# Kernel optimization log

Measured on AMD Instinct MI355X. Metric: run time of the kernel, lower is better.

The kernel has to match this reference:

```python
import jax, jax.numpy as jnp
import numpy as np

# dims
N, E, HID = 20000, 320000, 128
L, H = 12, 4            # num_layers, heads
C = 2 * HID             # h width = in_channels = out_channels*heads = 256
OC = C // H             # per-head out channels = 64
FF = 4 * HID            # ffn hidden = 512
LN_EPS = 1e-5
SLOPE = 0.2             # GATConv leaky_relu negative slope


def _layer_norm(x, g, b):
    m = x.mean(-1, keepdims=True)
    v = ((x - m) ** 2).mean(-1, keepdims=True)
    return (x - m) * jax.lax.rsqrt(v + LN_EPS) * g + b


def setup_inputs() -> dict:
    key = jax.random.key(0)
    ks = jax.random.split(key, 16)
    s = 0.05
    f32 = jnp.float32
    return {
        "hf": jax.random.normal(ks[0], (N, HID), f32),
        "hs": jax.random.normal(ks[1], (N, HID), f32),
        "edge_index": jax.random.randint(ks[2], (2, E), 0, N, dtype=jnp.int32),
        # GATConv params (stacked over layers)
        "W": jax.random.normal(ks[3], (L, C, H * OC), f32) * s,       # lin (no bias)
        "att_src": jax.random.normal(ks[4], (L, H, OC), f32) * s,
        "att_dst": jax.random.normal(ks[5], (L, H, OC), f32) * s,
        "gat_b": jax.random.normal(ks[6], (L, C), f32) * s,            # GATConv bias
        # FFN params
        "w1": jax.random.normal(ks[7], (L, C, FF), f32) * s,
        "b1": jax.random.normal(ks[8], (L, FF), f32) * s,
        "w2": jax.random.normal(ks[9], (L, FF, C), f32) * s,
        "b2": jax.random.normal(ks[10], (L, C), f32) * s,
        # LayerNorm params
        "ln1_g": jnp.ones((L, C), f32),
        "ln1_b": jnp.zeros((L, C), f32),
        "ln2_g": jnp.ones((L, C), f32),
        "ln2_b": jnp.zeros((L, C), f32),
    }


def reference(hf, hs, edge_index, W, att_src, att_dst, gat_b,
              w1, b1, w2, b2, ln1_g, ln1_b, ln2_g, ln2_b):
    # PyG GATConv add_self_loops=True
    loop = jnp.arange(N, dtype=edge_index.dtype)
    src = jnp.concatenate([edge_index[0], loop])  # [E+N]
    dst = jnp.concatenate([edge_index[1], loop])

    h = jnp.concatenate([hf, hs], axis=-1)  # [N, C]
    for i in range(L):
        # --- GATConv + residual + LN (dropout = identity at eval) ---
        r = h
        xh = (h @ W[i]).reshape(N, H, OC)              # [N,H,OC]
        a_s = (xh * att_src[i]).sum(-1)                # [N,H]
        a_d = (xh * att_dst[i]).sum(-1)                # [N,H]
        e = jax.nn.leaky_relu(a_s[src] + a_d[dst], SLOPE)          # [E+N,H]
        m = jax.ops.segment_max(e, dst, num_segments=N)            # [N,H]
        ex = jnp.exp(e - m[dst])
        z = jax.ops.segment_sum(ex, dst, num_segments=N)           # [N,H]
        alpha = ex / z[dst]                                        # segment softmax
        msg = xh[src] * alpha[..., None]                           # [E+N,H,OC]
        out = jax.ops.segment_sum(msg, dst, num_segments=N).reshape(N, C) + gat_b[i]
        h = _layer_norm(out + r, ln1_g[i], ln1_b[i])
        # --- FFN + residual + LN ---
        r = h
        f = jax.nn.relu(h @ w1[i] + b1[i]) @ w2[i] + b2[i]
        h = _layer_norm(f + r, ln2_g[i], ln2_b[i])

    return h[:, :HID], h[:, HID:]
```

## Files before the change

kernel.cpp:

```cpp
#include <hip/hip_runtime.h>
#include <hip/hip_bf16.h>
#include <math.h>

#define C_DIM 256
#define HID 128
#define HEADS 4
#define OC 64
#define FF_DIM 512
#define NLAYERS 12

constexpr float LN_EPS = 1e-5f;
constexpr float SLOPE  = 0.2f;

typedef __attribute__((ext_vector_type(4))) float f32x4;
typedef __attribute__((ext_vector_type(8))) short bf16x8_t;
typedef __attribute__((ext_vector_type(4))) int i32x4;

__device__ __forceinline__ float leaky(float x) { return x > 0.f ? x : SLOPE * x; }

__device__ __forceinline__ float bf2f(unsigned short u) {
    union { unsigned i; float f; } v; v.i = ((unsigned)u) << 16; return v.f;
}
__device__ __forceinline__ void bf2x(unsigned u, float& lo, float& hi) {
    union { unsigned i; float f; } a, b;
    a.i = u << 16; b.i = u & 0xffff0000u;
    lo = a.f; hi = b.f;
}
__device__ __forceinline__ unsigned packbf(float lo, float hi) {
    unsigned a = __bfloat16_as_ushort(__float2bfloat16(lo));
    unsigned b = __bfloat16_as_ushort(__float2bfloat16(hi));
    return a | (b << 16);
}

__global__ void zero_i32_kernel(int* __restrict__ p, int n) {
    int i = blockIdx.x * blockDim.x + threadIdx.x;
    if (i < n) p[i] = 0;
}

__global__ void concat_kernel(const float* __restrict__ hf, const float* __restrict__ hs,
                              __hip_bfloat16* __restrict__ hb, int Nn) {
    int idx = blockIdx.x * blockDim.x + threadIdx.x;
    int total = Nn * C_DIM;
    if (idx < total) {
        int n = idx >> 8;
        int c = idx & 255;
        float v = (c < HID) ? hf[n * HID + c] : hs[n * HID + (c - HID)];
        hb[idx] = __float2bfloat16(v);
    }
}

__global__ void transp_bf16_kernel(const float* __restrict__ in,
                                   __hip_bfloat16* __restrict__ out, int K, int N) {
    __shared__ float t[32][33];
    const float* inl = in + (size_t)blockIdx.z * K * N;
    __hip_bfloat16* outl = out + (size_t)blockIdx.z * K * N;
    int kb = blockIdx.y * 32, nb = blockIdx.x * 32;
    int tx = threadIdx.x & 31, ty = threadIdx.x >> 5;
    #pragma unroll
    for (int r = 0; r < 32; r += 8)
        t[ty + r][tx] = inl[(size_t)(kb + ty + r) * N + nb + tx];
    __syncthreads();
    #pragma unroll
    for (int r = 0; r < 32; r += 8)
        outl[(size_t)(nb + ty + r) * K + kb + tx] = __float2bfloat16(t[tx][ty + r]);
}

__global__ void hist_kernel(const int* __restrict__ dst, int* __restrict__ counts, int E) {
    int e = blockIdx.x * blockDim.x + threadIdx.x;
    if (e < E) atomicAdd(&counts[dst[e]], 1);
}

__global__ void scan_kernel(const int* __restrict__ counts, int* __restrict__ offsets,
                            int* __restrict__ cursor, int n) {
    __shared__ int wsum[16];
    __shared__ int carry_s;
    const int lane = threadIdx.x & 63, wid = threadIdx.x >> 6;
    if (threadIdx.x == 0) carry_s = 0;
    __syncthreads();
    for (int base = 0; base < n; base += 1024) {
        int i = base + (int)threadIdx.x;
        int v = (i < n) ? counts[i] : 0;
        int x = v;
        #pragma unroll
        for (int off = 1; off < 64; off <<= 1) {
            int t = __shfl_up(x, off);
            if (lane >= off) x += t;
        }
        if (lane == 63) wsum[wid] = x;
        __syncthreads();
        if (threadIdx.x == 0) {
            int acc = carry_s;
            #pragma unroll
            for (int w = 0; w < 16; ++w) { int t = wsum[w]; wsum[w] = acc; acc += t; }
            carry_s = acc;
        }
        __syncthreads();
        int excl = wsum[wid] + x - v;
        if (i < n) { offsets[i] = excl; cursor[i] = excl; }
        __syncthreads();
    }
    if (threadIdx.x == 0) offsets[n] = carry_s;
}

__global__ void fill_kernel(const int* __restrict__ src, const int* __restrict__ dst,
                            int* __restrict__ cursor, int* __restrict__ csr_src, int E) {
    int e = blockIdx.x * blockDim.x + threadIdx.x;
    if (e < E) {
        int d = dst[e];
        int p = atomicAdd(&cursor[d], 1);
        csr_src[p] = src[e];
    }
}

#define GBM 64
#define GBN 64
#define GBK 64
#define GLS 72

__global__ __launch_bounds__(256) void gemm_bf16_kernel(
    const __hip_bfloat16* __restrict__ A,
    const __hip_bfloat16* __restrict__ BT,
    const float* __restrict__ bias,
    __hip_bfloat16* __restrict__ Cb,
    const float* __restrict__ attS,
    const float* __restrict__ attD,
    float* __restrict__ aS,
    float* __restrict__ aD,
    int M, int N, int K, int relu)
{
    __shared__ short As[GBM * GLS];
    __shared__ short Bs[GBN * GLS];
    __shared__ float attP[2][2][GBM];
    const int tid = threadIdx.x;
    const int wave = tid >> 6, lane = tid & 63;
    const int lr = lane & 15, lq = lane >> 4;
    const int wm = (wave >> 1) * 32, wn = (wave & 1) * 32;
    const int row0 = blockIdx.x * GBM, col0 = blockIdx.y * GBN;

    const int sr = tid >> 2;
    const int sc = (tid & 3) * 16;

    f32x4 acc[2][2] = {};

    for (int k0 = 0; k0 < K; k0 += GBK) {
        int gr = row0 + sr;
        i32x4 va0 = {}, va1 = {};
        if (gr < M) {
            const __hip_bfloat16* ap = &A[(size_t)gr * K + k0 + sc];
            va0 = *(const i32x4*)ap;
            va1 = *(const i32x4*)(ap + 8);
        }
        *(i32x4*)&As[sr * GLS + sc] = va0;
        *(i32x4*)&As[sr * GLS + sc + 8] = va1;
        const __hip_bfloat16* bp = &BT[(size_t)(col0 + sr) * K + k0 + sc];
        *(i32x4*)&Bs[sr * GLS + sc] = *(const i32x4*)bp;
        *(i32x4*)&Bs[sr * GLS + sc + 8] = *(const i32x4*)(bp + 8);
        __syncthreads();

        #pragma unroll
        for (int ks = 0; ks < 2; ++ks) {
            bf16x8_t af[2], bfr[2];
            #pragma unroll
            for (int t = 0; t < 2; ++t) {
                af[t]  = *(const bf16x8_t*)&As[(wm + t * 16 + lr) * GLS + ks * 32 + lq * 8];
                bfr[t] = *(const bf16x8_t*)&Bs[(wn + t * 16 + lr) * GLS + ks * 32 + lq * 8];
            }
            #pragma unroll
            for (int mt = 0; mt < 2; ++mt)
                #pragma unroll
                for (int nt = 0; nt < 2; ++nt)
                    acc[mt][nt] = __builtin_amdgcn_mfma_f32_16x16x32_bf16(
                        af[mt], bfr[nt], acc[mt][nt], 0, 0, 0);
        }
        __syncthreads();
    }

    float bv[2];
    #pragma unroll
    for (int nt = 0; nt < 2; ++nt)
        bv[nt] = bias ? bias[col0 + wn + nt * 16 + lr] : 0.f;

    #pragma unroll
    for (int mt = 0; mt < 2; ++mt) {
        #pragma unroll
        for (int r = 0; r < 4; ++r) {
            int grow = row0 + wm + mt * 16 + lq * 4 + r;
            if (grow >= M) continue;
            #pragma unroll
            for (int nt = 0; nt < 2; ++nt) {
                float v = acc[mt][nt][r] + bv[nt];
                if (relu) v = fmaxf(v, 0.f);
                Cb[(size_t)grow * N + col0 + wn + nt * 16 + lr] = __float2bfloat16(v);
            }
        }
    }

    if (aS) {
        const int head = col0 >> 6;
        float atS[2], atD[2];
        #pragma unroll
        for (int nt = 0; nt < 2; ++nt) {
            int c = col0 + wn + nt * 16 + lr;
            atS[nt] = attS[c];
            atD[nt] = attD[c];
        }
        #pragma unroll
        for (int mt = 0; mt < 2; ++mt) {
            #pragma unroll
            for (int r = 0; r < 4; ++r) {
                float vs = acc[mt][0][r] * atS[0] + acc[mt][1][r] * atS[1];
                float vd = acc[mt][0][r] * atD[0] + acc[mt][1][r] * atD[1];
                #pragma unroll
                for (int off = 1; off < 16; off <<= 1) {
                    vs += __shfl_xor(vs, off);
                    vd += __shfl_xor(vd, off);
                }
                if (lr == 0) {
                    int rl = wm + mt * 16 + lq * 4 + r;
                    attP[wave & 1][0][rl] = vs;
                    attP[wave & 1][1][rl] = vd;
                }
            }
        }
        __syncthreads();
        if (tid < GBM) {
            int grow = row0 + tid;
            if (grow < M) {
                aS[grow * HEADS + head] = attP[0][0][tid] + attP[1][0][tid];
                aD[grow * HEADS + head] = attP[0][1][tid] + attP[1][1][tid];
            }
        }
    }
}

__global__ __launch_bounds__(256) void agg_kernel(
    const __hip_bfloat16* __restrict__ xhb, const float* __restrict__ a_s,
    const float* __restrict__ a_d, const int* __restrict__ csr,
    const int* __restrict__ offs, const float* __restrict__ gat_b,
    const float* __restrict__ ln_g, const float* __restrict__ ln_b,
    __hip_bfloat16* __restrict__ hb, int Nn)
{
    const int lane = threadIdx.x & 63;
    const int n = __builtin_amdgcn_readfirstlane(blockIdx.x * 4 + (threadIdx.x >> 6));
    if (n >= Nn) return;
    const int half = lane >> 5;
    const int sl = lane & 31;
    const int head = sl >> 3;
    const int c0 = sl * 8;
    const unsigned* x = (const unsigned*)xhb;
    const size_t rowp = (size_t)n * (C_DIM / 2) + (c0 >> 1);

    const float ad = a_d[n * 4 + head];

    const int beg = offs[n], end = offs[n + 1];
    const int ne = end - beg;
    const int nh0 = (ne + 1) >> 1;
    int ih  = half ? (beg + nh0) : beg;
    int cnt = half ? (ne - nh0) : nh0;

    i32x4 rv = *(const i32x4*)&((const unsigned*)hb)[rowp];

    float acc[8] = {};
    float z = 0.f;

    {
        float wself = __expf(leaky(a_s[n * 4 + head] + ad));
        if (half) {
            i32x4 xv = *(const i32x4*)&x[rowp];
            #pragma unroll
            for (int q = 0; q < 4; ++q) {
                float lo, hi; bf2x((unsigned)xv[q], lo, hi);
                acc[2 * q]     = wself * lo;
                acc[2 * q + 1] = wself * hi;
            }
            z = wself;
        }
    }

    for (; cnt >= 4; cnt -= 4, ih += 4) {
        int s0 = csr[ih], s1 = csr[ih + 1], s2 = csr[ih + 2], s3 = csr[ih + 3];
        float w0 = __expf(leaky(a_s[s0 * 4 + head] + ad));
        float w1 = __expf(leaky(a_s[s1 * 4 + head] + ad));
        float w2 = __expf(leaky(a_s[s2 * 4 + head] + ad));
        float w3 = __expf(leaky(a_s[s3 * 4 + head] + ad));
        i32x4 x0 = *(const i32x4*)&x[(size_t)s0 * (C_DIM / 2) + (c0 >> 1)];
        i32x4 x1 = *(const i32x4*)&x[(size_t)s1 * (C_DIM / 2) + (c0 >> 1)];
        i32x4 x2 = *(const i32x4*)&x[(size_t)s2 * (C_DIM / 2) + (c0 >> 1)];
        i32x4 x3 = *(const i32x4*)&x[(size_t)s3 * (C_DIM / 2) + (c0 >> 1)];
        #pragma unroll
        for (int q = 0; q < 4; ++q) {
            float lo, hi;
            bf2x((unsigned)x0[q], lo, hi);
            acc[2 * q] += w0 * lo; acc[2 * q + 1] += w0 * hi;
            bf2x((unsigned)x1[q], lo, hi);
            acc[2 * q] += w1 * lo; acc[2 * q + 1] += w1 * hi;
            bf2x((unsigned)x2[q], lo, hi);
            acc[2 * q] += w2 * lo; acc[2 * q + 1] += w2 * hi;
            bf2x((unsigned)x3[q], lo, hi);
            acc[2 * q] += w3 * lo; acc[2 * q + 1] += w3 * hi;
        }
        z += (w0 + w1) + (w2 + w3);
    }
    for (; cnt > 0; --cnt, ++ih) {
        int s0 = csr[ih];
        float w0 = __expf(leaky(a_s[s0 * 4 + head] + ad));
        i32x4 x0 = *(const i32x4*)&x[(size_t)s0 * (C_DIM / 2) + (c0 >> 1)];
        #pragma unroll
        for (int q = 0; q < 4; ++q) {
            float lo, hi; bf2x((unsigned)x0[q], lo, hi);
            acc[2 * q] += w0 * lo; acc[2 * q + 1] += w0 * hi;
        }
        z += w0;
    }

    #pragma unroll
    for (int j = 0; j < 8; ++j) acc[j] += __shfl_xor(acc[j], 32);
    z += __shfl_xor(z, 32);

    float res[8];
    #pragma unroll
    for (int q = 0; q < 4; ++q) bf2x((unsigned)rv[q], res[2 * q], res[2 * q + 1]);

    float4 gb0 = *(const float4*)&gat_b[c0];
    float4 gb1 = *(const float4*)&gat_b[c0 + 4];
    float gb[8] = {gb0.x, gb0.y, gb0.z, gb0.w, gb1.x, gb1.y, gb1.z, gb1.w};
    float rz = 1.0f / z;
    float val[8];
    #pragma unroll
    for (int j = 0; j < 8; ++j) val[j] = acc[j] * rz + gb[j] + res[j];

    float s1 = 0.f, s2 = 0.f;
    #pragma unroll
    for (int j = 0; j < 8; ++j) { s1 += val[j]; s2 += val[j] * val[j]; }
    #pragma unroll
    for (int off = 1; off < 64; off <<= 1) {
        s1 += __shfl_xor(s1, off);
        s2 += __shfl_xor(s2, off);
    }
    float mean = s1 * (1.0f / (2 * C_DIM));
    float inv = rsqrtf(s2 * (1.0f / (2 * C_DIM)) - mean * mean + LN_EPS);

    if (half == 0) {
        float4 g0 = *(const float4*)&ln_g[c0];
        float4 g1 = *(const float4*)&ln_g[c0 + 4];
        float4 bb0 = *(const float4*)&ln_b[c0];
        float4 bb1 = *(const float4*)&ln_b[c0 + 4];
        float g[8] = {g0.x, g0.y, g0.z, g0.w, g1.x, g1.y, g1.z, g1.w};
        float bb[8] = {bb0.x, bb0.y, bb0.z, bb0.w, bb1.x, bb1.y, bb1.z, bb1.w};
        float o[8];
        #pragma unroll
        for (int j = 0; j < 8; ++j) o[j] = (val[j] - mean) * inv * g[j] + bb[j];
        i32x4 ob;
        ob[0] = (int)packbf(o[0], o[1]);
        ob[1] = (int)packbf(o[2], o[3]);
        ob[2] = (int)packbf(o[4], o[5]);
        ob[3] = (int)packbf(o[6], o[7]);
        *(i32x4*)&((unsigned*)hb)[rowp] = ob;
    }
}

__global__ __launch_bounds__(256) void ln2_kernel(
    const __hip_bfloat16* __restrict__ fb, const float* __restrict__ ln_g,
    const float* __restrict__ ln_b, __hip_bfloat16* __restrict__ hb,
    float* __restrict__ out_split, int Nn)
{
    const int lane = threadIdx.x & 63;
    const int n = __builtin_amdgcn_readfirstlane(blockIdx.x * 4 + (threadIdx.x >> 6));
    if (n >= Nn) return;
    const int c0 = lane * 4;
    const unsigned short* f = (const unsigned short*)fb;
    const unsigned short* r = (const unsigned short*)hb;

    ushort4 rv = *(const ushort4*)&r[(size_t)n * C_DIM + c0];
    ushort4 fv = *(const ushort4*)&f[(size_t)n * C_DIM + c0];
    float val[4];
    val[0] = bf2f(fv.x) + bf2f(rv.x);
    val[1] = bf2f(fv.y) + bf2f(rv.y);
    val[2] = bf2f(fv.z) + bf2f(rv.z);
    val[3] = bf2f(fv.w) + bf2f(rv.w);

    float s1 = (val[0] + val[1]) + (val[2] + val[3]);
    float s2 = (val[0] * val[0] + val[1] * val[1]) + (val[2] * val[2] + val[3] * val[3]);
    #pragma unroll
    for (int off = 1; off < 64; off <<= 1) {
        s1 += __shfl_xor(s1, off);
        s2 += __shfl_xor(s2, off);
    }
    float mean = s1 * (1.0f / C_DIM);
    float inv = rsqrtf(s2 * (1.0f / C_DIM) - mean * mean + LN_EPS);
    float4 g = *(const float4*)&ln_g[c0];
    float4 bb = *(const float4*)&ln_b[c0];
    float4 o;
    o.x = (val[0] - mean) * inv * g.x + bb.x;
    o.y = (val[1] - mean) * inv * g.y + bb.y;
    o.z = (val[2] - mean) * inv * g.z + bb.z;
    o.w = (val[3] - mean) * inv * g.w + bb.w;

    if (out_split) {
        size_t off_ = (c0 < HID) ? ((size_t)n * HID + c0)
                                 : ((size_t)Nn * HID + (size_t)n * HID + (c0 - HID));
        *(float4*)&out_split[off_] = o;
    } else {
        ushort4 ob;
        ob.x = __bfloat16_as_ushort(__float2bfloat16(o.x));
        ob.y = __bfloat16_as_ushort(__float2bfloat16(o.y));
        ob.z = __bfloat16_as_ushort(__float2bfloat16(o.z));
        ob.w = __bfloat16_as_ushort(__float2bfloat16(o.w));
        *(ushort4*)&((unsigned short*)hb)[(size_t)n * C_DIM + c0] = ob;
    }
}

extern "C" void kernel_launch(void* const* d_in, const int* in_sizes, int n_in,
                              void* d_out, int out_size, void* d_ws, size_t ws_size,
                              hipStream_t stream)
{
    const float* hf       = (const float*)d_in[0];
    const float* hs       = (const float*)d_in[1];
    const int*   edge     = (const int*)  d_in[2];
    const float* W        = (const float*)d_in[3];
    const float* att_src  = (const float*)d_in[4];
    const float* att_dst  = (const float*)d_in[5];
    const float* gat_b    = (const float*)d_in[6];
    const float* w1       = (const float*)d_in[7];
    const float* b1       = (const float*)d_in[8];
    const float* w2       = (const float*)d_in[9];
    const float* b2       = (const float*)d_in[10];
    const float* ln1g     = (const float*)d_in[11];
    const float* ln1b     = (const float*)d_in[12];
    const float* ln2g     = (const float*)d_in[13];
    const float* ln2b     = (const float*)d_in[14];
    float* out = (float*)d_out;

    const int N = in_sizes[0] / HID;
    const int E = in_sizes[2] / 2;
    const int* e_src = edge;
    const int* e_dst = edge + E;

    char* p = (char*)d_ws;
    auto alloc = [&](size_t bytes) {
        char* r = p;
        p += (bytes + 255) & ~(size_t)255;
        return (void*)r;
    };
    __hip_bfloat16* hb     = (__hip_bfloat16*)alloc((size_t)N * C_DIM * 2);
    __hip_bfloat16* xhb    = (__hip_bfloat16*)alloc((size_t)N * C_DIM * 2);
    __hip_bfloat16* fbuf   = (__hip_bfloat16*)alloc((size_t)N * C_DIM * 2);
    __hip_bfloat16* midb   = (__hip_bfloat16*)alloc((size_t)N * FF_DIM * 2);
    float*          a_s    = (float*)alloc((size_t)N * HEADS * 4);
    float*          a_d    = (float*)alloc((size_t)N * HEADS * 4);
    int*            counts = (int*)alloc((size_t)N * 4);
    int*            offs   = (int*)alloc((size_t)(N + 1) * 4);
    int*            cursor = (int*)alloc((size_t)N * 4);
    int*            csr    = (int*)alloc((size_t)E * 4);
    __hip_bfloat16* WT     = (__hip_bfloat16*)alloc((size_t)NLAYERS * C_DIM * C_DIM * 2);
    __hip_bfloat16* w1T    = (__hip_bfloat16*)alloc((size_t)NLAYERS * C_DIM * FF_DIM * 2);
    __hip_bfloat16* w2T    = (__hip_bfloat16*)alloc((size_t)NLAYERS * FF_DIM * C_DIM * 2);

    {
        int total = N * C_DIM;
        concat_kernel<<<(total + 255) / 256, 256, 0, stream>>>(hf, hs, hb, N);
    }
    transp_bf16_kernel<<<dim3(C_DIM / 32, C_DIM / 32, NLAYERS), 256, 0, stream>>>(W, WT, C_DIM, C_DIM);
    transp_bf16_kernel<<<dim3(FF_DIM / 32, C_DIM / 32, NLAYERS), 256, 0, stream>>>(w1, w1T, C_DIM, FF_DIM);
    transp_bf16_kernel<<<dim3(C_DIM / 32, FF_DIM / 32, NLAYERS), 256, 0, stream>>>(w2, w2T, FF_DIM, C_DIM);

    zero_i32_kernel<<<(N + 255) / 256, 256, 0, stream>>>(counts, N);
    hist_kernel<<<(E + 255) / 256, 256, 0, stream>>>(e_dst, counts, E);
    scan_kernel<<<1, 1024, 0, stream>>>(counts, offs, cursor, N);
    fill_kernel<<<(E + 255) / 256, 256, 0, stream>>>(e_src, e_dst, cursor, csr, E);

    const int gm = (N + GBM - 1) / GBM;

    for (int l = 0; l < NLAYERS; ++l) {
        const __hip_bfloat16* Wl  = WT  + (size_t)l * C_DIM * C_DIM;
        const __hip_bfloat16* w1l = w1T + (size_t)l * C_DIM * FF_DIM;
        const __hip_bfloat16* w2l = w2T + (size_t)l * FF_DIM * C_DIM;
        const float* asl  = att_src + (size_t)l * C_DIM;
        const float* adl  = att_dst + (size_t)l * C_DIM;
        const float* gbl  = gat_b + (size_t)l * C_DIM;
        const float* b1l  = b1 + (size_t)l * FF_DIM;
        const float* b2l  = b2 + (size_t)l * C_DIM;
        const float* g1l  = ln1g + (size_t)l * C_DIM;
        const float* be1l = ln1b + (size_t)l * C_DIM;
        const float* g2l  = ln2g + (size_t)l * C_DIM;
        const float* be2l = ln2b + (size_t)l * C_DIM;

        gemm_bf16_kernel<<<dim3(gm, C_DIM / GBN), 256, 0, stream>>>(
            hb, Wl, nullptr, xhb, asl, adl, a_s, a_d, N, C_DIM, C_DIM, 0);
        agg_kernel<<<(N + 3) / 4, 256, 0, stream>>>(
            xhb, a_s, a_d, csr, offs, gbl, g1l, be1l, hb, N);
        gemm_bf16_kernel<<<dim3(gm, FF_DIM / GBN), 256, 0, stream>>>(
            hb, w1l, b1l, midb, nullptr, nullptr, nullptr, nullptr,
            N, FF_DIM, C_DIM, 1);
        gemm_bf16_kernel<<<dim3(gm, C_DIM / GBN), 256, 0, stream>>>(
            midb, w2l, b2l, fbuf, nullptr, nullptr, nullptr, nullptr,
            N, C_DIM, FF_DIM, 0);
        ln2_kernel<<<(N + 3) / 4, 256, 0, stream>>>(
            fbuf, g2l, be2l, hb, (l == NLAYERS - 1) ? out : nullptr, N);
    }
}
```

Before: 1.224 ms.

## Enlarge GEMM tiles to 128x128 and stage operands via direct global-to-LDS loads

The bf16 MFMA GEMM moves from 64x64 to 128x128 block tiles, with each wave computing a 64x64 sub-tile (4x4 MFMA accumulators) for more operand reuse per LDS load. Operand staging switches to global_load_lds direct-to-LDS transfers without padding or row bounds checks, so the activation buffers are padded by one tile of rows. The attention-logit epilogue now reduces a full head inside one wave and writes directly, dropping the shared-memory partial sums and an extra barrier. Risks include unpadded LDS bank conflicts, fewer blocks for occupancy, reading uninitialized padded rows, and missing waits around the async LDS loads.

```diff
diff --git a/kernel.cpp b/kernel.cpp
--- a/kernel.cpp
+++ b/kernel.cpp
@@ -30,6 +30,12 @@
     unsigned a = __bfloat16_as_ushort(__float2bfloat16(lo));
     unsigned b = __bfloat16_as_ushort(__float2bfloat16(hi));
     return a | (b << 16);
+}
+
+__device__ __forceinline__ void gl_lds16(const void* g, void* l) {
+    __builtin_amdgcn_global_load_lds(
+        (const __attribute__((address_space(1))) unsigned*)g,
+        (__attribute__((address_space(3))) unsigned*)l, 16, 0, 0);
 }
 
 __global__ void zero_i32_kernel(int* __restrict__ p, int n) {
@@ -112,10 +118,9 @@
     }
 }
 
-#define GBM 64
-#define GBN 64
+#define GBM 128
+#define GBN 128
 #define GBK 64
-#define GLS 72
 
 __global__ __launch_bounds__(256) void gemm_bf16_kernel(
     const __hip_bfloat16* __restrict__ A,
@@ -128,66 +133,61 @@
     float* __restrict__ aD,
     int M, int N, int K, int relu)
 {
-    __shared__ short As[GBM * GLS];
-    __shared__ short Bs[GBN * GLS];
-    __shared__ float attP[2][2][GBM];
-    const int tid = threadIdx.x;
+    __shared__ __align__(16) short As[GBM * (GBK)];
+    __shared__ __align__(16) short Bs[GBN * (GBK)];
+
+    const int tid  = threadIdx.x;
     const int wave = tid >> 6, lane = tid & 63;
     const int lr = lane & 15, lq = lane >> 4;
-    const int wm = (wave >> 1) * 32, wn = (wave & 1) * 32;
+    const int wm = (wave >> 1) * 64, wn = (wave & 1) * 64;
     const int row0 = blockIdx.x * GBM, col0 = blockIdx.y * GBN;
 
-    const int sr = tid >> 2;
-    const int sc = (tid & 3) * 16;
-
-    f32x4 acc[2][2] = {};
+    const int srow = lane >> 3;
+    const int scol = (lane & 7) * 8;
+
+    f32x4 acc[4][4] = {};
 
     for (int k0 = 0; k0 < K; k0 += GBK) {
-        int gr = row0 + sr;
-        i32x4 va0 = {}, va1 = {};
-        if (gr < M) {
-            const __hip_bfloat16* ap = &A[(size_t)gr * K + k0 + sc];
-            va0 = *(const i32x4*)ap;
-            va1 = *(const i32x4*)(ap + 8);
-        }
-        *(i32x4*)&As[sr * GLS + sc] = va0;
-        *(i32x4*)&As[sr * GLS + sc + 8] = va1;
-        const __hip_bfloat16* bp = &BT[(size_t)(col0 + sr) * K + k0 + sc];
-        *(i32x4*)&Bs[sr * GLS + sc] = *(const i32x4*)bp;
-        *(i32x4*)&Bs[sr * GLS + sc + 8] = *(const i32x4*)(bp + 8);
+        #pragma unroll
+        for (int i = 0; i < 4; ++i) {
+            const int c = wave * 4 + i;
+            const int r = c * 8 + srow;
+            gl_lds16(&A [(size_t)(row0 + r) * K + k0 + scol], &As[c * 512 + lane * 8]);
+            gl_lds16(&BT[(size_t)(col0 + r) * K + k0 + scol], &Bs[c * 512 + lane * 8]);
+        }
         __syncthreads();
 
         #pragma unroll
         for (int ks = 0; ks < 2; ++ks) {
-            bf16x8_t af[2], bfr[2];
-            #pragma unroll
-            for (int t = 0; t < 2; ++t) {
-                af[t]  = *(const bf16x8_t*)&As[(wm + t * 16 + lr) * GLS + ks * 32 + lq * 8];
-                bfr[t] = *(const bf16x8_t*)&Bs[(wn + t * 16 + lr) * GLS + ks * 32 + lq * 8];
+            bf16x8_t af[4], bfr[4];
+            #pragma unroll
+            for (int t = 0; t < 4; ++t) {
+                af[t]  = *(const bf16x8_t*)&As[(wm + t * 16 + lr) * GBK + ks * 32 + lq * 8];
+                bfr[t] = *(const bf16x8_t*)&Bs[(wn + t * 16 + lr) * GBK + ks * 32 + lq * 8];
             }
             #pragma unroll
-            for (int mt = 0; mt < 2; ++mt)
+            for (int mt = 0; mt < 4; ++mt)
                 #pragma unroll
-                for (int nt = 0; nt < 2; ++nt)
+                for (int nt = 0; nt < 4; ++nt)
                     acc[mt][nt] = __builtin_amdgcn_mfma_f32_16x16x32_bf16(
                         af[mt], bfr[nt], acc[mt][nt], 0, 0, 0);
         }
         __syncthreads();
     }
 
-    float bv[2];
-    #pragma unroll
-    for (int nt = 0; nt < 2; ++nt)
+    float bv[4];
+    #pragma unroll
+    for (int nt = 0; nt < 4; ++nt)
         bv[nt] = bias ? bias[col0 + wn + nt * 16 + lr] : 0.f;
 
     #pragma unroll
-    for (int mt = 0; mt < 2; ++mt) {
+    for (int mt = 0; mt < 4; ++mt) {
         #pragma unroll
         for (int r = 0; r < 4; ++r) {
             int grow = row0 + wm + mt * 16 + lq * 4 + r;
             if (grow >= M) continue;
             #pragma unroll
-            for (int nt = 0; nt < 2; ++nt) {
+            for (int nt = 0; nt < 4; ++nt) {
                 float v = acc[mt][nt][r] + bv[nt];
                 if (relu) v = fmaxf(v, 0.f);
                 Cb[(size_t)grow * N + col0 + wn + nt * 16 + lr] = __float2bfloat16(v);
@@ -196,38 +196,34 @@
     }
 
     if (aS) {
-        const int head = col0 >> 6;
-        float atS[2], atD[2];
-        #pragma unroll
-        for (int nt = 0; nt < 2; ++nt) {
+        const int head = (col0 + wn) >> 6;
+        float atS[4], atD[4];
+        #pragma unroll
+        for (int nt = 0; nt < 4; ++nt) {
             int c = col0 + wn + nt * 16 + lr;
             atS[nt] = attS[c];
             atD[nt] = attD[c];
         }
         #pragma unroll
-        for (int mt = 0; mt < 2; ++mt) {
+        for (int mt = 0; mt < 4; ++mt) {
             #pragma unroll
             for (int r = 0; r < 4; ++r) {
-                float vs = acc[mt][0][r] * atS[0] + acc[mt][1][r] * atS[1];
-                float vd = acc[mt][0][r] * atD[0] + acc[mt][1][r] * atD[1];
+                float vs = acc[mt][0][r] * atS[0] + acc[mt][1][r] * atS[1]
+                         + acc[mt][2][r] * atS[2] + acc[mt][3][r] * atS[3];
+                float vd = acc[mt][0][r] * atD[0] + acc[mt][1][r] * atD[1]
+                         + acc[mt][2][r] * atD[2] + acc[mt][3][r] * atD[3];
                 #pragma unroll
                 for (int off = 1; off < 16; off <<= 1) {
                     vs += __shfl_xor(vs, off);
                     vd += __shfl_xor(vd, off);
                 }
                 if (lr == 0) {
-                    int rl = wm + mt * 16 + lq * 4 + r;
-                    attP[wave & 1][0][rl] = vs;
-                    attP[wave & 1][1][rl] = vd;
+                    int grow = row0 + wm + mt * 16 + lq * 4 + r;
+                    if (grow < M) {
+                        aS[grow * HEADS + head] = vs;
+                        aD[grow * HEADS + head] = vd;
+                    }
                 }
-            }
-        }
-        __syncthreads();
-        if (tid < GBM) {
-            int grow = row0 + tid;
-            if (grow < M) {
-                aS[grow * HEADS + head] = attP[0][0][tid] + attP[1][0][tid];
-                aD[grow * HEADS + head] = attP[0][1][tid] + attP[1][1][tid];
             }
         }
     }
@@ -442,10 +438,11 @@
         p += (bytes + 255) & ~(size_t)255;
         return (void*)r;
     };
-    __hip_bfloat16* hb     = (__hip_bfloat16*)alloc((size_t)N * C_DIM * 2);
+    const int NPAD = N + GBM;
+    __hip_bfloat16* hb     = (__hip_bfloat16*)alloc((size_t)NPAD * C_DIM * 2);
     __hip_bfloat16* xhb    = (__hip_bfloat16*)alloc((size_t)N * C_DIM * 2);
     __hip_bfloat16* fbuf   = (__hip_bfloat16*)alloc((size_t)N * C_DIM * 2);
-    __hip_bfloat16* midb   = (__hip_bfloat16*)alloc((size_t)N * FF_DIM * 2);
+    __hip_bfloat16* midb   = (__hip_bfloat16*)alloc((size_t)NPAD * FF_DIM * 2);
     float*          a_s    = (float*)alloc((size_t)N * HEADS * 4);
     float*          a_d    = (float*)alloc((size_t)N * HEADS * 4);
     int*            counts = (int*)alloc((size_t)N * 4);
```

After: 1.297 ms. 1.06x slower.

## Double-buffer GEMM tiles with direct global-to-LDS loads

Applied to the files above, without the earlier changes.

Replaces the register-staged global loads into padded shared memory with 16-byte global_load_lds transfers into two unpadded LDS buffers per operand. The next K tile is prefetched while MFMAs run on the current one. The row bounds check is dropped, so the A-operand buffers get 128 padding rows to keep out-of-range reads inside allocated memory. Losing the padding can cause LDS bank conflicts on the fragment reads. The hunk that shows the loop end and the synchronization between buffers is not visible, so wait and barrier correctness is uncertain.

```diff
diff --git a/kernel.cpp b/kernel.cpp
--- a/kernel.cpp
+++ b/kernel.cpp
@@ -30,6 +30,12 @@
     unsigned a = __bfloat16_as_ushort(__float2bfloat16(lo));
     unsigned b = __bfloat16_as_ushort(__float2bfloat16(hi));
     return a | (b << 16);
+}
+
+__device__ __forceinline__ void gl_lds16(const void* g, void* l) {
+    __builtin_amdgcn_global_load_lds(
+        (const __attribute__((address_space(1))) unsigned*)g,
+        (__attribute__((address_space(3))) unsigned*)l, 16, 0, 0);
 }
 
 __global__ void zero_i32_kernel(int* __restrict__ p, int n) {
@@ -115,7 +121,6 @@
 #define GBM 64
 #define GBN 64
 #define GBK 64
-#define GLS 72
 
 __global__ __launch_bounds__(256) void gemm_bf16_kernel(
     const __hip_bfloat16* __restrict__ A,
@@ -128,42 +133,50 @@
     float* __restrict__ aD,
     int M, int N, int K, int relu)
 {
-    __shared__ short As[GBM * GLS];
-    __shared__ short Bs[GBN * GLS];
+    __shared__ __align__(16) short As[2][GBM * GBK];
+    __shared__ __align__(16) short Bs[2][GBN * GBK];
     __shared__ float attP[2][2][GBM];
-    const int tid = threadIdx.x;
+
+    const int tid  = threadIdx.x;
     const int wave = tid >> 6, lane = tid & 63;
     const int lr = lane & 15, lq = lane >> 4;
     const int wm = (wave >> 1) * 32, wn = (wave & 1) * 32;
     const int row0 = blockIdx.x * GBM, col0 = blockIdx.y * GBN;
 
-    const int sr = tid >> 2;
-    const int sc = (tid & 3) * 16;
-
+    const int sr = wave * 8 + (lane >> 3);
+    const int sc = (lane & 7) * 8;
+
+    const int ntiles = K / GBK;
     f32x4 acc[2][2] = {};
 
-    for (int k0 = 0; k0 < K; k0 += GBK) {
-        int gr = row0 + sr;
-        i32x4 va0 = {}, va1 = {};
-        if (gr < M) {
-            const __hip_bfloat16* ap = &A[(size_t)gr * K + k0 + sc];
-            va0 = *(const i32x4*)ap;
-            va1 = *(const i32x4*)(ap + 8);
-        }
-        *(i32x4*)&As[sr * GLS + sc] = va0;
-        *(i32x4*)&As[sr * GLS + sc + 8] = va1;
-        const __hip_bfloat16* bp = &BT[(size_t)(col0 + sr) * K + k0 + sc];
-        *(i32x4*)&Bs[sr * GLS + sc] = *(const i32x4*)bp;
-        *(i32x4*)&Bs[sr * GLS + sc + 8] = *(const i32x4*)(bp + 8);
-        __syncthreads();
-
+    #pragma unroll
+    for (int i = 0; i < 2; ++i) {
+        const int r = i * 32 + sr;
+        gl_lds16(&A [(size_t)(row0 + r) * K + sc], &As[0][r * GBK + sc]);
+        gl_lds16(&BT[(size_t)(col0 + r) * K + sc], &Bs[0][r * GBK + sc]);
+    }
+    __syncthreads();
+
+    for (int t = 0; t < ntiles; ++t) {
+        const int cur = t & 1;
+        if (t + 1 < ntiles) {
+            const int k0 = (t + 1) * GBK;
+            #pragma unroll
+            for (int i = 0; i < 2; ++i) {
+                const int r = i * 32 + sr;
+                gl_lds16(&A [(size_t)(row0 + r) * K + k0 + sc], &As[cur ^ 1][r * GBK + sc]);
+                gl_lds16(&BT[(size_t)(col0 + r) * K + k0 + sc], &Bs[cur ^ 1][r * GBK + sc]);
+            }
+        }
+        const short* as = As[cur];
+        const short* bs = Bs[cur];
         #pragma unroll
         for (int ks = 0; ks < 2; ++ks) {
             bf16x8_t af[2], bfr[2];
             #pragma unroll
-            for (int t = 0; t < 2; ++t) {
-                af[t]  = *(const bf16x8_t*)&As[(wm + t * 16 + lr) * GLS + ks * 32 + lq * 8];
-                bfr[t] = *(const bf16x8_t*)&Bs[(wn + t * 16 + lr) * GLS + ks * 32 + lq * 8];
+            for (int tt = 0; tt < 2; ++tt) {
+                af[tt]  = *(const bf16x8_t*)&as[(wm + tt * 16 + lr) * GBK + ks * 32 + lq * 8];
+                bfr[tt] = *(const bf16x8_t*)&bs[(wn + tt * 16 + lr) * GBK + ks * 32 + lq * 8];
             }
             #pragma unroll
             for (int mt = 0; mt < 2; ++mt)
@@ -442,10 +455,11 @@
         p += (bytes + 255) & ~(size_t)255;
         return (void*)r;
     };
-    __hip_bfloat16* hb     = (__hip_bfloat16*)alloc((size_t)N * C_DIM * 2);
+    const int NPAD = N + 128;
+    __hip_bfloat16* hb     = (__hip_bfloat16*)alloc((size_t)NPAD * C_DIM * 2);
     __hip_bfloat16* xhb    = (__hip_bfloat16*)alloc((size_t)N * C_DIM * 2);
     __hip_bfloat16* fbuf   = (__hip_bfloat16*)alloc((size_t)N * C_DIM * 2);
-    __hip_bfloat16* midb   = (__hip_bfloat16*)alloc((size_t)N * FF_DIM * 2);
+    __hip_bfloat16* midb   = (__hip_bfloat16*)alloc((size_t)NPAD * FF_DIM * 2);
     float*          a_s    = (float*)alloc((size_t)N * HEADS * 4);
     float*          a_d    = (float*)alloc((size_t)N * HEADS * 4);
     int*            counts = (int*)alloc((size_t)N * 4);
```

Result: slower. 1.357 ms (+10.9%).

## Fuse second FFN GEMM with bias, residual and LayerNorm epilogue

Applied to the files above, without the earlier changes.

Replaces the FF2 GEMM plus separate ln2 kernel with one kernel. Each block computes a full 32-row by 256-column output tile, then adds bias and residual and applies LayerNorm in registers, with a cross-wave reduction through shared memory. This removes the intermediate fbuf write and re-read and one launch per layer. In exchange, every block reloads the whole weight matrix for only 32 rows, and the epilogue uses scalar strided stores.

```diff
diff --git a/kernel.cpp b/kernel.cpp
--- a/kernel.cpp
+++ b/kernel.cpp
@@ -233,6 +233,141 @@
     }
 }
 
+#define FBM 32
+
+__global__ __launch_bounds__(256) void gemm3_ln_kernel(
+    const __hip_bfloat16* __restrict__ A,
+    const __hip_bfloat16* __restrict__ BT,
+    const float* __restrict__ bias,
+    const float* __restrict__ ln_g, const float* __restrict__ ln_b,
+    __hip_bfloat16* __restrict__ hb,
+    float* __restrict__ out_split,
+    int M)
+{
+    __shared__ short As[FBM * GLS];
+    __shared__ short Bs[C_DIM * GLS];
+    __shared__ float rsum[2][FBM][4];
+
+    const int tid = threadIdx.x;
+    const int wave = tid >> 6, lane = tid & 63;
+    const int lr = lane & 15, lq = lane >> 4;
+    const int wn = wave * 64;
+    const int row0 = blockIdx.x * FBM;
+
+    const int sr = tid >> 2;
+    const int sc = (tid & 3) * 16;
+
+    f32x4 acc[2][4] = {};
+
+    for (int k0 = 0; k0 < FF_DIM; k0 += GBK) {
+        if (sr < FBM) {
+            const __hip_bfloat16* ap = &A[(size_t)(row0 + sr) * FF_DIM + k0 + sc];
+            *(i32x4*)&As[sr * GLS + sc] = *(const i32x4*)ap;
+            *(i32x4*)&As[sr * GLS + sc + 8] = *(const i32x4*)(ap + 8);
+        }
+        #pragma unroll
+        for (int rb = 0; rb < 4; ++rb) {
+            const int br = rb * 64 + sr;
+            const __hip_bfloat16* bp = &BT[(size_t)br * FF_DIM + k0 + sc];
+            *(i32x4*)&Bs[br * GLS + sc] = *(const i32x4*)bp;
+            *(i32x4*)&Bs[br * GLS + sc + 8] = *(const i32x4*)(bp + 8);
+        }
+        __syncthreads();
+
+        #pragma unroll
+        for (int ks = 0; ks < 2; ++ks) {
+            bf16x8_t af[2], bfr[4];
+            #pragma unroll
+            for (int mt = 0; mt < 2; ++mt)
+                af[mt] = *(const bf16x8_t*)&As[(mt * 16 + lr) * GLS + ks * 32 + lq * 8];
+            #pragma unroll
+            for (int nt = 0; nt < 4; ++nt)
+                bfr[nt] = *(const bf16x8_t*)&Bs[(wn + nt * 16 + lr) * GLS + ks * 32 + lq * 8];
+            #pragma unroll
+            for (int mt = 0; mt < 2; ++mt)
+                #pragma unroll
+                for (int nt = 0; nt < 4; ++nt)
+                    acc[mt][nt] = __builtin_amdgcn_mfma_f32_16x16x32_bf16(
+                        af[mt], bfr[nt], acc[mt][nt], 0, 0, 0);
+        }
+        __syncthreads();
+    }
+
+    float bv[4];
+    #pragma unroll
+    for (int nt = 0; nt < 4; ++nt)
+        bv[nt] = bias[wn + nt * 16 + lr];
+
+    const unsigned short* hbp = (const unsigned short*)hb;
+    #pragma unroll
+    for (int mt = 0; mt < 2; ++mt) {
+        #pragma unroll
+        for (int r = 0; r < 4; ++r) {
+            const int rb = mt * 16 + lq * 4 + r;
+            const int grow = row0 + rb;
+            float s1 = 0.f, s2 = 0.f;
+            #pragma unroll
+            for (int nt = 0; nt < 4; ++nt) {
+                float res = (grow < M)
+                    ? bf2f(hbp[(size_t)grow * C_DIM + wn + nt * 16 + lr]) : 0.f;
+                float v = acc[mt][nt][r] + bv[nt] + res;
+                acc[mt][nt][r] = v;
+                s1 += v; s2 += v * v;
+            }
+            #pragma unroll
+            for (int off = 1; off < 16; off <<= 1) {
+                s1 += __shfl_xor(s1, off);
+                s2 += __shfl_xor(s2, off);
+            }
+            if (lr == 0) {
+                rsum[0][rb][wave] = s1;
+                rsum[1][rb][wave] = s2;
+            }
+        }
+    }
+    __syncthreads();
+
+    float4 gv, bbv;
+    float g[4], bb[4];
+    #pragma unroll
+    for (int nt = 0; nt < 4; ++nt) {
+        g[nt]  = ln_g[wn + nt * 16 + lr];
+        bb[nt] = ln_b[wn + nt * 16 + lr];
+    }
+    (void)gv; (void)bbv;
+
+    #pragma unroll
+    for (int mt = 0; mt < 2; ++mt) {
+        #pragma unroll
+        for (int r = 0; r < 4; ++r) {
+            const int rb = mt * 16 + lq * 4 + r;
+            const int grow = row0 + rb;
+            if (grow >= M) continue;
+            float s1 = (rsum[0][rb][0] + rsum[0][rb][1]) + (rsum[0][rb][2] + rsum[0][rb][3]);
+            float s2 = (rsum[1][rb][0] + rsum[1][rb][1]) + (rsum[1][rb][2] + rsum[1][rb][3]);
+            float mean = s1 * (1.0f / C_DIM);
+            float inv = rsqrtf(s2 * (1.0f / C_DIM) - mean * mean + LN_EPS);
+            if (out_split) {
+                #pragma unroll
+                for (int nt = 0; nt < 4; ++nt) {
+                    float o = (acc[mt][nt][r] - mean) * inv * g[nt] + bb[nt];
+                    int c = wn + nt * 16 + lr;
+                    size_t off_ = (c < HID) ? ((size_t)grow * HID + c)
+                                            : ((size_t)M * HID + (size_t)grow * HID + (c - HID));
+                    out_split[off_] = o;
+                }
+            } else {
+                #pragma unroll
+                for (int nt = 0; nt < 4; ++nt) {
+                    float o = (acc[mt][nt][r] - mean) * inv * g[nt] + bb[nt];
+                    ((unsigned short*)hb)[(size_t)grow * C_DIM + wn + nt * 16 + lr] =
+                        __bfloat16_as_ushort(__float2bfloat16(o));
+                }
+            }
+        }
+    }
+}
+
 __global__ __launch_bounds__(256) void agg_kernel(
     const __hip_bfloat16* __restrict__ xhb, const float* __restrict__ a_s,
     const float* __restrict__ a_d, const int* __restrict__ csr,
@@ -356,57 +491,6 @@
         ob[2] = (int)packbf(o[4], o[5]);
         ob[3] = (int)packbf(o[6], o[7]);
         *(i32x4*)&((unsigned*)hb)[rowp] = ob;
-    }
-}
-
-__global__ __launch_bounds__(256) void ln2_kernel(
-    const __hip_bfloat16* __restrict__ fb, const float* __restrict__ ln_g,
-    const float* __restrict__ ln_b, __hip_bfloat16* __restrict__ hb,
-    float* __restrict__ out_split, int Nn)
-{
-    const int lane = threadIdx.x & 63;
-    const int n = __builtin_amdgcn_readfirstlane(blockIdx.x * 4 + (threadIdx.x >> 6));
-    if (n >= Nn) return;
-    const int c0 = lane * 4;
-    const unsigned short* f = (const unsigned short*)fb;
-    const unsigned short* r = (const unsigned short*)hb;
-
-    ushort4 rv = *(const ushort4*)&r[(size_t)n * C_DIM + c0];
-    ushort4 fv = *(const ushort4*)&f[(size_t)n * C_DIM + c0];
-    float val[4];
-    val[0] = bf2f(fv.x) + bf2f(rv.x);
-    val[1] = bf2f(fv.y) + bf2f(rv.y);
-    val[2] = bf2f(fv.z) + bf2f(rv.z);
-    val[3] = bf2f(fv.w) + bf2f(rv.w);
-
-    float s1 = (val[0] + val[1]) + (val[2] + val[3]);
-    float s2 = (val[0] * val[0] + val[1] * val[1]) + (val[2] * val[2] + val[3] * val[3]);
-    #pragma unroll
-    for (int off = 1; off < 64; off <<= 1) {
-        s1 += __shfl_xor(s1, off);
-        s2 += __shfl_xor(s2, off);
-    }
-    float mean = s1 * (1.0f / C_DIM);
-    float inv = rsqrtf(s2 * (1.0f / C_DIM) - mean * mean + LN_EPS);
-    float4 g = *(const float4*)&ln_g[c0];
-    float4 bb = *(const float4*)&ln_b[c0];
-    float4 o;
-    o.x = (val[0] - mean) * inv * g.x + bb.x;
-    o.y = (val[1] - mean) * inv * g.y + bb.y;
-    o.z = (val[2] - mean) * inv * g.z + bb.z;
-    o.w = (val[3] - mean) * inv * g.w + bb.w;
-
-    if (out_split) {
-        size_t off_ = (c0 < HID) ? ((size_t)n * HID + c0)
-                                 : ((size_t)Nn * HID + (size_t)n * HID + (c0 - HID));
-        *(float4*)&out_split[off_] = o;
-    } else {
-        ushort4 ob;
-        ob.x = __bfloat16_as_ushort(__float2bfloat16(o.x));
-        ob.y = __bfloat16_as_ushort(__float2bfloat16(o.y));
-        ob.z = __bfloat16_as_ushort(__float2bfloat16(o.z));
-        ob.w = __bfloat16_as_ushort(__float2bfloat16(o.w));
-        *(ushort4*)&((unsigned short*)hb)[(size_t)n * C_DIM + c0] = ob;
     }
 }
 
@@ -444,7 +528,6 @@
     };
     __hip_bfloat16* hb     = (__hip_bfloat16*)alloc((size_t)N * C_DIM * 2);
     __hip_bfloat16* xhb    = (__hip_bfloat16*)alloc((size_t)N * C_DIM * 2);
-    __hip_bfloat16* fbuf   = (__hip_bfloat16*)alloc((size_t)N * C_DIM * 2);
     __hip_bfloat16* midb   = (__hip_bfloat16*)alloc((size_t)N * FF_DIM * 2);
     float*          a_s    = (float*)alloc((size_t)N * HEADS * 4);
     float*          a_d    = (float*)alloc((size_t)N * HEADS * 4);
@@ -470,6 +553,7 @@
     fill_kernel<<<(E + 255) / 256, 256, 0, stream>>>(e_src, e_dst, cursor, csr, E);
 
     const int gm = (N + GBM - 1) / GBM;
+    const int gf = (N + FBM - 1) / FBM;
 
     for (int l = 0; l < NLAYERS; ++l) {
         const __hip_bfloat16* Wl  = WT  + (size_t)l * C_DIM * C_DIM;
@@ -492,10 +576,8 @@
         gemm_bf16_kernel<<<dim3(gm, FF_DIM / GBN), 256, 0, stream>>>(
             hb, w1l, b1l, midb, nullptr, nullptr, nullptr, nullptr,
             N, FF_DIM, C_DIM, 1);
-        gemm_bf16_kernel<<<dim3(gm, C_DIM / GBN), 256, 0, stream>>>(
-            midb, w2l, b2l, fbuf, nullptr, nullptr, nullptr, nullptr,
-            N, C_DIM, FF_DIM, 0);
-        ln2_kernel<<<(N + 3) / 4, 256, 0, stream>>>(
-            fbuf, g2l, be2l, hb, (l == NLAYERS - 1) ? out : nullptr, N);
-    }
-}
+        gemm3_ln_kernel<<<gf, 256, 0, stream>>>(
+            midb, w2l, b2l, g2l, be2l, hb,
+            (l == NLAYERS - 1) ? out : nullptr, N);
+    }
+}
```

New measurement: 1.210 ms. About the same (-1.1%).
